# Performance work log

Hardware: AMD Instinct MI355X
Metric: run time of the kernel (lower is better)

## Reference

```python
import jax, jax.numpy as jnp
import numpy as np

S, H, I, E, K = 32, 768, 768, 32, 4
LIMIT = 7.0
ALPHA = 1.702
EPS = 1e-5


def setup_inputs() -> dict:
    key = jax.random.key(0)
    ks = jax.random.split(key, 8)
    return {
        "x": jax.random.normal(ks[0], (S, H), dtype=jnp.float32),
        "norm_scale": jnp.ones((H,), dtype=jnp.float32),
        "gate_w": jax.random.normal(ks[1], (E, H), dtype=jnp.float32) * 0.02,
        "gate_b": jnp.zeros((E,), dtype=jnp.float32),
        "w1": jax.random.normal(ks[2], (E, 2 * I, H), dtype=jnp.float32) * 0.02,
        "b1": jax.random.normal(ks[3], (E, 2 * I), dtype=jnp.float32) * 0.02,
        "w2": jax.random.normal(ks[4], (E, H, I), dtype=jnp.float32) * 0.02,
        "b2": jax.random.normal(ks[5], (E, H), dtype=jnp.float32) * 0.02,
    }


def reference(x, norm_scale, gate_w, gate_b, w1, b1, w2, b2):
    # RMSNorm
    t = x * jax.lax.rsqrt(jnp.mean(x * x, axis=-1, keepdims=True) + EPS) * norm_scale
    # Router: top-k experts per token, softmax over the k selected logits
    g = t @ gate_w.T + gate_b                      # (S, E)
    vals, idx = jax.lax.top_k(g, K)                # (S, K)
    expert_weights = jax.nn.softmax(vals, axis=-1)  # (S, K)
    # Per-token expert weight gather (irregular access, as in load_experts)
    mw1 = w1[idx]                                  # (S, K, 2I, H)
    mb1 = b1[idx]                                  # (S, K, 2I)
    h = jnp.einsum('beck,bk->bec', mw1, t) + mb1   # (S, K, 2I)
    # Interleaved SwiGLU with clamp limit (gpt-oss style)
    x_glu = jnp.minimum(h[..., ::2], LIMIT)
    x_lin = jnp.clip(h[..., 1::2], -LIMIT, LIMIT)
    act = x_glu * jax.nn.sigmoid(ALPHA * x_glu) * (x_lin + 1.0)  # (S, K, I)
    mw2 = w2[idx]                                  # (S, K, H, I)
    mb2 = b2[idx]                                  # (S, K, H)
    o = jnp.einsum('beck,bek->bec', mw2, act) + mb2  # (S, K, H)
    t_out = jnp.einsum('bec,be->bc', o, expert_weights)  # (S, H)
    return x + t_out
```

## Files before the change

### kernel.cpp

```cpp
#include <hip/hip_runtime.h>

#define S 32
#define H 768
#define IDIM 768
#define E 32
#define K 4
#define TWO_I 1536
#define LIMIT 7.0f
#define ALPHA 1.702f
#define EPS 1e-5f
#define CHUNK 8

__device__ inline float dot4(float4 a, float4 b) {
  return a.x*b.x + a.y*b.y + a.z*b.z + a.w*b.w;
}

__device__ inline float coreduce4(float a0, float a1, float a2, float a3, int lane) {
  const bool hi32 = (lane & 32) != 0;
  float s0 = hi32 ? a2 : a0;
  float o0 = hi32 ? a0 : a2;
  float s1 = hi32 ? a3 : a1;
  float o1 = hi32 ? a1 : a3;
  s0 += __shfl_xor(o0, 32);
  s1 += __shfl_xor(o1, 32);
  const bool hi16 = (lane & 16) != 0;
  float u  = hi16 ? s1 : s0;
  float ov = hi16 ? s0 : s1;
  u += __shfl_xor(ov, 16);
  u += __shfl_xor(u, 8);
  u += __shfl_xor(u, 4);
  u += __shfl_xor(u, 2);
  u += __shfl_xor(u, 1);
  return u;
}

__global__ void k_norm_router(const float* __restrict__ x,
                              const float* __restrict__ norm_scale,
                              const float* __restrict__ gate_w,
                              const float* __restrict__ gate_b,
                              float* __restrict__ t_out,
                              float* __restrict__ wt_out,
                              int* __restrict__ idx_out) {
  __shared__ float t_s[H];
  __shared__ float red_s[4];
  __shared__ float logit_s[E];
  const int b = blockIdx.x;
  const int tid = threadIdx.x;
  const int lane = tid & 63, wave = tid >> 6;

  float v0 = x[b*H + tid];
  float v1 = x[b*H + tid + 256];
  float v2 = x[b*H + tid + 512];
  float ss = v0*v0 + v1*v1 + v2*v2;
#pragma unroll
  for (int o = 32; o; o >>= 1) ss += __shfl_xor(ss, o);
  if (lane == 0) red_s[wave] = ss;
  __syncthreads();
  float mean = (red_s[0] + red_s[1] + red_s[2] + red_s[3]) * (1.0f/(float)H) + EPS;
  float rs = rsqrtf(mean);
  rs = rs * (1.5f - 0.5f*mean*rs*rs);
  float t0 = v0*rs*norm_scale[tid];
  float t1 = v1*rs*norm_scale[tid+256];
  float t2 = v2*rs*norm_scale[tid+512];
  t_s[tid] = t0; t_s[tid+256] = t1; t_s[tid+512] = t2;
  t_out[b*H+tid] = t0; t_out[b*H+tid+256] = t1; t_out[b*H+tid+512] = t2;
  __syncthreads();

  for (int e = wave; e < E; e += 4) {
    const float* gw = gate_w + e*H;
    float s = 0.f;
#pragma unroll
    for (int j = 0; j < H/64; ++j) {
      int p = lane + j*64;
      s += gw[p] * t_s[p];
    }
#pragma unroll
    for (int o = 32; o; o >>= 1) s += __shfl_xor(s, o);
    if (lane == 0) logit_s[e] = s + gate_b[e];
  }
  __syncthreads();

  if (tid == 0) {
    float lg[E];
    for (int e = 0; e < E; ++e) lg[e] = logit_s[e];
    float vals[K]; int idxs[K];
    for (int k = 0; k < K; ++k) {
      float best = -3.4e38f; int bi = 0;
      for (int e = 0; e < E; ++e)
        if (lg[e] > best) { best = lg[e]; bi = e; }
      vals[k] = best; idxs[k] = bi; lg[bi] = -3.4e38f;
    }
    float m = vals[0], sum = 0.f, w[K];
    for (int k = 0; k < K; ++k) { w[k] = expf(vals[k]-m); sum += w[k]; }
    float inv = 1.f/sum;
    for (int k = 0; k < K; ++k) {
      wt_out[b*K+k] = w[k]*inv;
      idx_out[b*K+k] = idxs[k];
    }
  }
}

#define BUILD_LIST(eexpr)                                                   \
  if (tid < 64) {                                                           \
    int a0 = idx_all[tid];                                                  \
    int a1 = idx_all[tid + 64];                                             \
    unsigned long long m0 = __ballot(a0 == (eexpr));                        \
    unsigned long long m1 = __ballot(a1 == (eexpr));                        \
    unsigned long long below = (1ULL << tid) - 1ULL;                        \
    if (a0 == (eexpr)) list_s[__popcll(m0 & below)] = tid;                  \
    if (a1 == (eexpr)) list_s[__popcll(m0) + __popcll(m1 & below)] = tid + 64; \
    if (tid == 0) n_s = (int)(__popcll(m0) + __popcll(m1));                 \
  }                                                                         \
  __syncthreads();

__global__ void k_gemv1(const float* __restrict__ w1,
                        const float* __restrict__ b1,
                        const float* __restrict__ t,
                        const int* __restrict__ idx_all,
                        float* __restrict__ act) {
  const int e = blockIdx.x;
  const int tid = threadIdx.x;
  const int lane = tid & 63, wave = tid >> 6;
  __shared__ float t_lds[CHUNK*H];
  __shared__ float h_lds[32*CHUNK];
  __shared__ int list_s[S];
  __shared__ int n_s;

  BUILD_LIST(e)
  const int n = n_s;
  if (n == 0) return;
  const int row0 = blockIdx.y * 32;

  for (int c0 = 0; c0 < n; c0 += CHUNK) {
    const int cn = min(CHUNK, n - c0);
    for (int q = tid; q < cn*(H/4); q += 256) {
      int j = q / (H/4), p = q - j*(H/4);
      int bt = list_s[c0+j] >> 2;
      ((float4*)(t_lds + j*H))[p] = ((const float4*)(t + (size_t)bt*H))[p];
    }
    __syncthreads();

#pragma unroll
    for (int rt4 = 0; rt4 < 2; ++rt4) {
      const int lrow = wave*8 + rt4*4;
      const int r = row0 + lrow;
      float4 wv[4][3]; float bias[4];
#pragma unroll
      for (int rr = 0; rr < 4; ++rr) {
        const float4* row = (const float4*)(w1 + ((size_t)e*TWO_I + r + rr)*H);
        wv[rr][0] = row[lane]; wv[rr][1] = row[lane+64]; wv[rr][2] = row[lane+128];
        bias[rr] = b1[(size_t)e*TWO_I + r + rr];
      }
      for (int j = 0; j < cn; ++j) {
        const float4* tv = (const float4*)(t_lds + j*H);
        float4 x0 = tv[lane], x1 = tv[lane+64], x2 = tv[lane+128];
        float a0 = dot4(wv[0][0],x0) + dot4(wv[0][1],x1) + dot4(wv[0][2],x2);
        float a1 = dot4(wv[1][0],x0) + dot4(wv[1][1],x1) + dot4(wv[1][2],x2);
        float a2 = dot4(wv[2][0],x0) + dot4(wv[2][1],x1) + dot4(wv[2][2],x2);
        float a3 = dot4(wv[3][0],x0) + dot4(wv[3][1],x1) + dot4(wv[3][2],x2);
        float u = coreduce4(a0, a1, a2, a3, lane);
        const bool hi32 = (lane & 32) != 0, hi16 = (lane & 16) != 0;
        float bsel = hi32 ? (hi16 ? bias[3] : bias[2]) : (hi16 ? bias[1] : bias[0]);
        if ((lane & 15) == 0)
          h_lds[(lrow + (lane >> 4))*CHUNK + j] = u + bsel;
      }
    }
    __syncthreads();

    for (int q = tid; q < 16*cn; q += 256) {
      int c = q & 15, j = q >> 4;
      float he = h_lds[(2*c)*CHUNK + j];
      float ho = h_lds[(2*c+1)*CHUNK + j];
      float xg = fminf(he, LIMIT);
      float xl = fminf(fmaxf(ho, -LIMIT), LIMIT);
      float sig = 1.f/(1.f + expf(-ALPHA*xg));
      int aid = list_s[c0 + j];
      act[(size_t)aid*IDIM + (row0 >> 1) + c] = xg*sig*(xl + 1.f);
    }
    __syncthreads();
  }
}

__global__ void k_gemv2(const float* __restrict__ w2,
                        const float* __restrict__ b2,
                        const float* __restrict__ act,
                        const int* __restrict__ idx_all,
                        float* __restrict__ o) {
  const int e = blockIdx.x;
  const int tid = threadIdx.x;
  const int lane = tid & 63, wave = tid >> 6;
  __shared__ float a_lds[CHUNK*IDIM];
  __shared__ float o_lds[16*CHUNK];
  __shared__ int list_s[S];
  __shared__ int n_s;

  BUILD_LIST(e)
  const int n = n_s;
  if (n == 0) return;
  const int row0 = blockIdx.y * 16;

  for (int c0 = 0; c0 < n; c0 += CHUNK) {
    const int cn = min(CHUNK, n - c0);
    for (int q = tid; q < cn*(IDIM/4); q += 256) {
      int j = q / (IDIM/4), p = q - j*(IDIM/4);
      int aid = list_s[c0+j];
      ((float4*)(a_lds + j*IDIM))[p] = ((const float4*)(act + (size_t)aid*IDIM))[p];
    }
    __syncthreads();

    {
      const int lrow = wave*4;
      const int r = row0 + lrow;
      float4 wv[4][3]; float bias[4];
#pragma unroll
      for (int rr = 0; rr < 4; ++rr) {
        const float4* row = (const float4*)(w2 + ((size_t)e*H + r + rr)*IDIM);
        wv[rr][0] = row[lane]; wv[rr][1] = row[lane+64]; wv[rr][2] = row[lane+128];
        bias[rr] = b2[(size_t)e*H + r + rr];
      }
      for (int j = 0; j < cn; ++j) {
        const float4* tv = (const float4*)(a_lds + j*IDIM);
        float4 x0 = tv[lane], x1 = tv[lane+64], x2 = tv[lane+128];
        float a0 = dot4(wv[0][0],x0) + dot4(wv[0][1],x1) + dot4(wv[0][2],x2);
        float a1 = dot4(wv[1][0],x0) + dot4(wv[1][1],x1) + dot4(wv[1][2],x2);
        float a2 = dot4(wv[2][0],x0) + dot4(wv[2][1],x1) + dot4(wv[2][2],x2);
        float a3 = dot4(wv[3][0],x0) + dot4(wv[3][1],x1) + dot4(wv[3][2],x2);
        float u = coreduce4(a0, a1, a2, a3, lane);
        const bool hi32 = (lane & 32) != 0, hi16 = (lane & 16) != 0;
        float bsel = hi32 ? (hi16 ? bias[3] : bias[2]) : (hi16 ? bias[1] : bias[0]);
        if ((lane & 15) == 0)
          o_lds[(lrow + (lane >> 4))*CHUNK + j] = u + bsel;
      }
    }
    __syncthreads();

    for (int q = tid; q < 16*cn; q += 256) {
      int rl = q & 15, j = q >> 4;
      int aid = list_s[c0 + j];
      o[(size_t)aid*H + row0 + rl] = o_lds[rl*CHUNK + j];
    }
    __syncthreads();
  }
}

__global__ void k_finalize(const float* __restrict__ x,
                           const float* __restrict__ o,
                           const float* __restrict__ wt,
                           float* __restrict__ out) {
  int g = blockIdx.x*256 + threadIdx.x;
  int b = g / H;
  int c = g - b*H;
  float acc = x[g];
#pragma unroll
  for (int k = 0; k < K; ++k)
    acc += wt[b*K + k] * o[(size_t)(b*K + k)*H + c];
  out[g] = acc;
}

extern "C" void kernel_launch(void* const* d_in, const int* in_sizes, int n_in,
                              void* d_out, int out_size, void* d_ws, size_t ws_size,
                              hipStream_t stream) {
  const float* x          = (const float*)d_in[0];
  const float* norm_scale = (const float*)d_in[1];
  const float* gate_w     = (const float*)d_in[2];
  const float* gate_b     = (const float*)d_in[3];
  const float* w1         = (const float*)d_in[4];
  const float* b1         = (const float*)d_in[5];
  const float* w2         = (const float*)d_in[6];
  const float* b2         = (const float*)d_in[7];
  float* out = (float*)d_out;

  float* t       = (float*)d_ws;
  float* wt      = t + S*H;
  int*   idx_all = (int*)(wt + S*K);
  float* act     = (float*)(idx_all + S*K);
  float* o       = act + S*K*IDIM;

  k_norm_router<<<S, 256, 0, stream>>>(x, norm_scale, gate_w, gate_b,
                                       t, wt, idx_all);
  dim3 g1(E, TWO_I/32);
  k_gemv1<<<g1, 256, 0, stream>>>(w1, b1, t, idx_all, act);
  dim3 g2(E, H/16);
  k_gemv2<<<g2, 256, 0, stream>>>(w2, b2, act, idx_all, o);
  k_finalize<<<(S*H)/256, 256, 0, stream>>>(x, o, wt, out);
}
```

Before: 312.1 us.

## Fuse finalize into gemv2 via atomics and prefetch weights before routing list

The router kernel now writes x into the output as the residual base. gemv2 atomically adds weighted expert outputs straight into it, so the o buffer and the finalize kernel go away. Both GEMV kernels now load their weight rows into registers before building the token list, and gemv1 halves its rows per block to double the grid. This overlaps weight loads with the routing setup and cuts a launch, but the float atomics make the sum order nondeterministic and add contention, and experts with no tokens still load their weights.

```diff
diff --git a/kernel.cpp b/kernel.cpp
--- a/kernel.cpp
+++ b/kernel.cpp
@@ -34,13 +34,15 @@
   return u;
 }
 
-__global__ void k_norm_router(const float* __restrict__ x,
-                              const float* __restrict__ norm_scale,
-                              const float* __restrict__ gate_w,
-                              const float* __restrict__ gate_b,
-                              float* __restrict__ t_out,
-                              float* __restrict__ wt_out,
-                              int* __restrict__ idx_out) {
+__global__ __launch_bounds__(256)
+void k_norm_router(const float* __restrict__ x,
+                   const float* __restrict__ norm_scale,
+                   const float* __restrict__ gate_w,
+                   const float* __restrict__ gate_b,
+                   float* __restrict__ t_out,
+                   float* __restrict__ wt_out,
+                   int* __restrict__ idx_out,
+                   float* __restrict__ out) {
   __shared__ float t_s[H];
   __shared__ float red_s[4];
   __shared__ float logit_s[E];
@@ -51,6 +53,9 @@
   float v0 = x[b*H + tid];
   float v1 = x[b*H + tid + 256];
   float v2 = x[b*H + tid + 512];
+  out[b*H + tid]       = v0;
+  out[b*H + tid + 256] = v1;
+  out[b*H + tid + 512] = v2;
   float ss = v0*v0 + v1*v1 + v2*v2;
 #pragma unroll
   for (int o = 32; o; o >>= 1) ss += __shfl_xor(ss, o);
@@ -113,23 +118,34 @@
   }                                                                         \
   __syncthreads();
 
-__global__ void k_gemv1(const float* __restrict__ w1,
-                        const float* __restrict__ b1,
-                        const float* __restrict__ t,
-                        const int* __restrict__ idx_all,
-                        float* __restrict__ act) {
+__global__ __launch_bounds__(256)
+void k_gemv1(const float* __restrict__ w1,
+             const float* __restrict__ b1,
+             const float* __restrict__ t,
+             const int* __restrict__ idx_all,
+             float* __restrict__ act) {
   const int e = blockIdx.x;
   const int tid = threadIdx.x;
   const int lane = tid & 63, wave = tid >> 6;
+  const int row0 = blockIdx.y * 16;
+  const int r = row0 + wave*4;
+
+  float4 wv[4][3]; float bias[4];
+#pragma unroll
+  for (int rr = 0; rr < 4; ++rr) {
+    const float4* row = (const float4*)(w1 + ((size_t)e*TWO_I + r + rr)*H);
+    wv[rr][0] = row[lane]; wv[rr][1] = row[lane+64]; wv[rr][2] = row[lane+128];
+    bias[rr] = b1[(size_t)e*TWO_I + r + rr];
+  }
+
   __shared__ float t_lds[CHUNK*H];
-  __shared__ float h_lds[32*CHUNK];
+  __shared__ float h_lds[16*CHUNK];
   __shared__ int list_s[S];
   __shared__ int n_s;
 
   BUILD_LIST(e)
   const int n = n_s;
   if (n == 0) return;
-  const int row0 = blockIdx.y * 32;
 
   for (int c0 = 0; c0 < n; c0 += CHUNK) {
     const int cn = min(CHUNK, n - c0);
@@ -140,35 +156,23 @@
     }
     __syncthreads();
 
-#pragma unroll
-    for (int rt4 = 0; rt4 < 2; ++rt4) {
-      const int lrow = wave*8 + rt4*4;
-      const int r = row0 + lrow;
-      float4 wv[4][3]; float bias[4];
-#pragma unroll
-      for (int rr = 0; rr < 4; ++rr) {
-        const float4* row = (const float4*)(w1 + ((size_t)e*TWO_I + r + rr)*H);
-        wv[rr][0] = row[lane]; wv[rr][1] = row[lane+64]; wv[rr][2] = row[lane+128];
-        bias[rr] = b1[(size_t)e*TWO_I + r + rr];
-      }
-      for (int j = 0; j < cn; ++j) {
-        const float4* tv = (const float4*)(t_lds + j*H);
-        float4 x0 = tv[lane], x1 = tv[lane+64], x2 = tv[lane+128];
-        float a0 = dot4(wv[0][0],x0) + dot4(wv[0][1],x1) + dot4(wv[0][2],x2);
-        float a1 = dot4(wv[1][0],x0) + dot4(wv[1][1],x1) + dot4(wv[1][2],x2);
-        float a2 = dot4(wv[2][0],x0) + dot4(wv[2][1],x1) + dot4(wv[2][2],x2);
-        float a3 = dot4(wv[3][0],x0) + dot4(wv[3][1],x1) + dot4(wv[3][2],x2);
-        float u = coreduce4(a0, a1, a2, a3, lane);
-        const bool hi32 = (lane & 32) != 0, hi16 = (lane & 16) != 0;
-        float bsel = hi32 ? (hi16 ? bias[3] : bias[2]) : (hi16 ? bias[1] : bias[0]);
-        if ((lane & 15) == 0)
-          h_lds[(lrow + (lane >> 4))*CHUNK + j] = u + bsel;
-      }
-    }
-    __syncthreads();
-
-    for (int q = tid; q < 16*cn; q += 256) {
-      int c = q & 15, j = q >> 4;
+    for (int j = 0; j < cn; ++j) {
+      const float4* tv = (const float4*)(t_lds + j*H);
+      float4 x0 = tv[lane], x1 = tv[lane+64], x2 = tv[lane+128];
+      float a0 = dot4(wv[0][0],x0) + dot4(wv[0][1],x1) + dot4(wv[0][2],x2);
+      float a1 = dot4(wv[1][0],x0) + dot4(wv[1][1],x1) + dot4(wv[1][2],x2);
+      float a2 = dot4(wv[2][0],x0) + dot4(wv[2][1],x1) + dot4(wv[2][2],x2);
+      float a3 = dot4(wv[3][0],x0) + dot4(wv[3][1],x1) + dot4(wv[3][2],x2);
+      float u = coreduce4(a0, a1, a2, a3, lane);
+      const bool hi32 = (lane & 32) != 0, hi16 = (lane & 16) != 0;
+      float bsel = hi32 ? (hi16 ? bias[3] : bias[2]) : (hi16 ? bias[1] : bias[0]);
+      if ((lane & 15) == 0)
+        h_lds[(wave*4 + (lane >> 4))*CHUNK + j] = u + bsel;
+    }
+    __syncthreads();
+
+    for (int q = tid; q < 8*cn; q += 256) {
+      int c = q & 7, j = q >> 3;
       float he = h_lds[(2*c)*CHUNK + j];
       float ho = h_lds[(2*c+1)*CHUNK + j];
       float xg = fminf(he, LIMIT);
@@ -181,23 +185,34 @@
   }
 }
 
-__global__ void k_gemv2(const float* __restrict__ w2,
-                        const float* __restrict__ b2,
-                        const float* __restrict__ act,
-                        const int* __restrict__ idx_all,
-                        float* __restrict__ o) {
+__global__ __launch_bounds__(256)
+void k_gemv2(const float* __restrict__ w2,
+             const float* __restrict__ b2,
+             const float* __restrict__ act,
+             const int* __restrict__ idx_all,
+             const float* __restrict__ wt,
+             float* __restrict__ out) {
   const int e = blockIdx.x;
   const int tid = threadIdx.x;
   const int lane = tid & 63, wave = tid >> 6;
+  const int row0 = blockIdx.y * 16;
+  const int r = row0 + wave*4;
+
+  float4 wv[4][3]; float bias[4];
+#pragma unroll
+  for (int rr = 0; rr < 4; ++rr) {
+    const float4* row = (const float4*)(w2 + ((size_t)e*H + r + rr)*IDIM);
+    wv[rr][0] = row[lane]; wv[rr][1] = row[lane+64]; wv[rr][2] = row[lane+128];
+    bias[rr] = b2[(size_t)e*H + r + rr];
+  }
+
   __shared__ float a_lds[CHUNK*IDIM];
-  __shared__ float o_lds[16*CHUNK];
   __shared__ int list_s[S];
   __shared__ int n_s;
 
   BUILD_LIST(e)
   const int n = n_s;
   if (n == 0) return;
-  const int row0 = blockIdx.y * 16;
 
   for (int c0 = 0; c0 < n; c0 += CHUNK) {
     const int cn = min(CHUNK, n - c0);
@@ -208,53 +223,24 @@
     }
     __syncthreads();
 
-    {
-      const int lrow = wave*4;
-      const int r = row0 + lrow;
-      float4 wv[4][3]; float bias[4];
-#pragma unroll
-      for (int rr = 0; rr < 4; ++rr) {
-        const float4* row = (const float4*)(w2 + ((size_t)e*H + r + rr)*IDIM);
-        wv[rr][0] = row[lane]; wv[rr][1] = row[lane+64]; wv[rr][2] = row[lane+128];
-        bias[rr] = b2[(size_t)e*H + r + rr];
+    for (int j = 0; j < cn; ++j) {
+      const float4* tv = (const float4*)(a_lds + j*IDIM);
+      float4 x0 = tv[lane], x1 = tv[lane+64], x2 = tv[lane+128];
+      float a0 = dot4(wv[0][0],x0) + dot4(wv[0][1],x1) + dot4(wv[0][2],x2);
+      float a1 = dot4(wv[1][0],x0) + dot4(wv[1][1],x1) + dot4(wv[1][2],x2);
+      float a2 = dot4(wv[2][0],x0) + dot4(wv[2][1],x1) + dot4(wv[2][2],x2);
+      float a3 = dot4(wv[3][0],x0) + dot4(wv[3][1],x1) + dot4(wv[3][2],x2);
+      float u = coreduce4(a0, a1, a2, a3, lane);
+      const bool hi32 = (lane & 32) != 0, hi16 = (lane & 16) != 0;
+      float bsel = hi32 ? (hi16 ? bias[3] : bias[2]) : (hi16 ? bias[1] : bias[0]);
+      if ((lane & 15) == 0) {
+        int aid = list_s[c0 + j];
+        int bt = aid >> 2;
+        atomicAdd(&out[bt*H + r + (lane >> 4)], wt[aid] * (u + bsel));
       }
-      for (int j = 0; j < cn; ++j) {
-        const float4* tv = (const float4*)(a_lds + j*IDIM);
-        float4 x0 = tv[lane], x1 = tv[lane+64], x2 = tv[lane+128];
-        float a0 = dot4(wv[0][0],x0) + dot4(wv[0][1],x1) + dot4(wv[0][2],x2);
-        float a1 = dot4(wv[1][0],x0) + dot4(wv[1][1],x1) + dot4(wv[1][2],x2);
-        float a2 = dot4(wv[2][0],x0) + dot4(wv[2][1],x1) + dot4(wv[2][2],x2);
-        float a3 = dot4(wv[3][0],x0) + dot4(wv[3][1],x1) + dot4(wv[3][2],x2);
-        float u = coreduce4(a0, a1, a2, a3, lane);
-        const bool hi32 = (lane & 32) != 0, hi16 = (lane & 16) != 0;
-        float bsel = hi32 ? (hi16 ? bias[3] : bias[2]) : (hi16 ? bias[1] : bias[0]);
-        if ((lane & 15) == 0)
-          o_lds[(lrow + (lane >> 4))*CHUNK + j] = u + bsel;
-      }
-    }
-    __syncthreads();
-
-    for (int q = tid; q < 16*cn; q += 256) {
-      int rl = q & 15, j = q >> 4;
-      int aid = list_s[c0 + j];
-      o[(size_t)aid*H + row0 + rl] = o_lds[rl*CHUNK + j];
-    }
-    __syncthreads();
-  }
-}
-
-__global__ void k_finalize(const float* __restrict__ x,
-                           const float* __restrict__ o,
-                           const float* __restrict__ wt,
-                           float* __restrict__ out) {
-  int g = blockIdx.x*256 + threadIdx.x;
-  int b = g / H;
-  int c = g - b*H;
-  float acc = x[g];
-#pragma unroll
-  for (int k = 0; k < K; ++k)
-    acc += wt[b*K + k] * o[(size_t)(b*K + k)*H + c];
-  out[g] = acc;
+    }
+    __syncthreads();
+  }
 }
 
 extern "C" void kernel_launch(void* const* d_in, const int* in_sizes, int n_in,
@@ -274,13 +260,11 @@
   float* wt      = t + S*H;
   int*   idx_all = (int*)(wt + S*K);
   float* act     = (float*)(idx_all + S*K);
-  float* o       = act + S*K*IDIM;
 
   k_norm_router<<<S, 256, 0, stream>>>(x, norm_scale, gate_w, gate_b,
-                                       t, wt, idx_all);
-  dim3 g1(E, TWO_I/32);
+                                       t, wt, idx_all, out);
+  dim3 g1(E, TWO_I/16);
   k_gemv1<<<g1, 256, 0, stream>>>(w1, b1, t, idx_all, act);
   dim3 g2(E, H/16);
-  k_gemv2<<<g2, 256, 0, stream>>>(w2, b2, act, idx_all, o);
-  k_finalize<<<(S*H)/256, 256, 0, stream>>>(x, o, wt, out);
-}
+  k_gemv2<<<g2, 256, 0, stream>>>(w2, b2, act, idx_all, wt, out);
+}
```

New measurement: 303.5 us. -2.7%, faster.
